# Kernel optimization log

Measured on AMD Instinct MI355X. Metric: run time of the kernel, lower is better.

Reference implementation:

```python
import jax, jax.numpy as jnp
import numpy as np

D = 1024   # embed_dim
H = 16     # n_heads
DH = D // H
B, N = 4, 1024


def setup_inputs() -> dict:
    key = jax.random.key(0)
    k0, k1, k2 = jax.random.split(key, 3)
    x = jax.random.normal(k0, (B, N, D), jnp.float32)
    # Per-head kqv Linear weights batched: each head maps D -> 2*D + D//H
    Wkqv = jax.random.normal(k1, (H, D, 2 * D + DH), jnp.float32) * 0.02
    bkqv = jnp.zeros((H, 2 * D + DH), jnp.float32)
    Wp = jax.random.normal(k2, (D, D), jnp.float32) * 0.02
    bp = jnp.zeros((D,), jnp.float32)
    return {"x": x, "Wkqv": Wkqv, "bkqv": bkqv, "Wp": Wp, "bp": bp}


def reference(x, Wkqv, bkqv, Wp, bp):
    Bm, Nm, Dm = x.shape
    # batched per-head projections: y[b,h,n,:] = x[b,n,:] @ Wkqv[h] + bkqv[h]
    y = jnp.einsum('bnd,hde->bhne', x, Wkqv) + bkqv[None, :, None, :]
    k = y[..., :Dm]          # [B,H,N,D]  (full embed_dim per head, as in source)
    q = y[..., Dm:2 * Dm]    # [B,H,N,D]
    v = y[..., 2 * Dm:]      # [B,H,N,DH]
    # attention_scores: q @ k^T / sqrt(D) -- scale uses FULL embed_dim (faithful)
    A = jnp.einsum('bhnd,bhmd->bhnm', q, k) / jnp.sqrt(jnp.float32(Dm))
    mask = jnp.tril(jnp.ones((Nm, Nm), dtype=bool))
    A = jnp.where(mask[None, None], A, -jnp.inf)
    A = jax.nn.softmax(A, axis=-1)
    sa = jnp.einsum('bhnm,bhmd->bnhd', A, v).reshape(Bm, Nm, Dm)
    return sa @ Wp + bp
```

## Files before the change

kernel.cpp:

```cpp
#include <hip/hip_runtime.h>
#include <hip/hip_bf16.h>

#define B_ 4
#define N_ 1024
#define D_ 1024
#define H_ 16
#define DH_ 64
#define E_ 2112
#define ROWS_ 4096

typedef __bf16 bf16_t;
typedef bf16_t bf16x4 __attribute__((ext_vector_type(4)));
typedef bf16_t bf16x8 __attribute__((ext_vector_type(8)));
typedef float f32x4 __attribute__((ext_vector_type(4)));

__device__ __forceinline__ void gload_lds16(const void* g, void* l) {
  __builtin_amdgcn_global_load_lds(
      (const __attribute__((address_space(1))) void*)g,
      (__attribute__((address_space(3))) void*)l, 16, 0, 0);
}

__global__ __launch_bounds__(256)
void prep_all(const float* __restrict__ x, const float* __restrict__ Wp,
              const float* __restrict__ W, const float* __restrict__ bkqv,
              bf16_t* __restrict__ xb, bf16_t* __restrict__ Wpt,
              bf16_t* __restrict__ Wvt, float* __restrict__ bqk) {
  __shared__ float smem[1056];
  const int bid = blockIdx.x;
  const int t = threadIdx.x;
  if (bid < 1024) {
    const int n4 = ROWS_ * D_ / 4;
    for (int i = bid * 256 + t; i < n4; i += 1024 * 256) {
      float4 v = ((const float4*)x)[i];
      bf16x4 o = {(bf16_t)v.x, (bf16_t)v.y, (bf16_t)v.z, (bf16_t)v.w};
      ((bf16x4*)xb)[i] = o;
    }
  } else if (bid < 2048) {
    const int id = bid - 1024;
    const int nt = id & 31, kt = id >> 5;
    const int tx = t & 31, ty = t >> 5;
    #pragma unroll
    for (int rr = 0; rr < 4; ++rr)
      smem[(rr * 8 + ty) * 33 + tx] =
          Wp[(size_t)(kt * 32 + rr * 8 + ty) * D_ + nt * 32 + tx];
    __syncthreads();
    #pragma unroll
    for (int rr = 0; rr < 4; ++rr)
      Wpt[(size_t)(nt * 32 + rr * 8 + ty) * D_ + kt * 32 + tx] =
          (bf16_t)smem[tx * 33 + rr * 8 + ty];
  } else if (bid < 3072) {
    const int id = bid - 2048;
    const int et = id & 1, dt = (id >> 1) & 31, h = id >> 6;
    const int tx = t & 31, ty = t >> 5;
    const float* Wh = W + (size_t)h * D_ * E_;
    #pragma unroll
    for (int rr = 0; rr < 4; ++rr) {
      int d = dt * 32 + rr * 8 + ty;
      int dh = et * 32 + tx;
      smem[(rr * 8 + ty) * 33 + tx] = Wh[(size_t)d * E_ + 2048 + dh];
    }
    __syncthreads();
    bf16_t* Wvo = Wvt + (size_t)h * DH_ * D_;
    #pragma unroll
    for (int rr = 0; rr < 4; ++rr) {
      int dh = et * 32 + rr * 8 + ty;
      int d = dt * 32 + tx;
      Wvo[(size_t)dh * D_ + d] = (bf16_t)smem[tx * 33 + rr * 8 + ty];
    }
  } else {
    const int h = bid - 3072;
    const float* bk = bkqv + h * E_;
    const float* bq = bk + 1024;
    float4 a = *(const float4*)(bk + t * 4);
    float4 b = *(const float4*)(bq + t * 4);
    smem[t] = a.x * b.x + a.y * b.y + a.z * b.z + a.w * b.w;
    __syncthreads();
    for (int st = 128; st > 0; st >>= 1) {
      if (t < st) smem[t] += smem[t + st];
      __syncthreads();
    }
    if (t == 0) bqk[h] = smem[0];
  }
}

__global__ __launch_bounds__(256)
void conv_wqk(const float* __restrict__ W, const float* __restrict__ bkqv,
              bf16_t* __restrict__ Wqb, bf16_t* __restrict__ Wkb,
              float* __restrict__ wqbk, float* __restrict__ wkbq) {
  const int db = blockIdx.x;
  const int h = blockIdx.y;
  const float* Wh = W + (size_t)h * D_ * E_;
  __shared__ float bq[1024], bk[1024];
  __shared__ float red[2][16][17];
  const int t = threadIdx.x;
  for (int i = t; i < 1024; i += 256) {
    bk[i] = bkqv[h * E_ + i];
    bq[i] = bkqv[h * E_ + 1024 + i];
  }
  __syncthreads();
  const int rt = t >> 4, ct = t & 15;
  const int d = db * 16 + rt;
  const float* rowp = Wh + (size_t)d * E_;
  float pk = 0.f, pq = 0.f;
  #pragma unroll
  for (int j = 0; j < 16; ++j) {
    int e4 = (ct + j * 16) * 4;
    float4 vk = *(const float4*)(rowp + e4);
    float4 vq = *(const float4*)(rowp + 1024 + e4);
    bf16x4 ok = {(bf16_t)vk.x, (bf16_t)vk.y, (bf16_t)vk.z, (bf16_t)vk.w};
    bf16x4 oq = {(bf16_t)vq.x, (bf16_t)vq.y, (bf16_t)vq.z, (bf16_t)vq.w};
    *(bf16x4*)(Wkb + ((size_t)h * 1024 + d) * 1024 + e4) = ok;
    *(bf16x4*)(Wqb + ((size_t)h * 1024 + d) * 1024 + e4) = oq;
    pk += vk.x * bq[e4] + vk.y * bq[e4 + 1] + vk.z * bq[e4 + 2] + vk.w * bq[e4 + 3];
    pq += vq.x * bk[e4] + vq.y * bk[e4 + 1] + vq.z * bk[e4 + 2] + vq.w * bk[e4 + 3];
  }
  red[0][rt][ct] = pk;
  red[1][rt][ct] = pq;
  __syncthreads();
  if (t < 32) {
    int which = t >> 4, r = t & 15;
    float s = 0.f;
    #pragma unroll
    for (int c2 = 0; c2 < 16; ++c2) s += red[which][r][c2];
    if (which == 0) wkbq[h * 1024 + db * 16 + r] = s;
    else            wqbk[h * 1024 + db * 16 + r] = s;
  }
}

__global__ __launch_bounds__(256)
void uv_kernel(const float* __restrict__ x, const float* __restrict__ bqk,
               const float* __restrict__ wqbk, const float* __restrict__ wkbq,
               float* __restrict__ u, float* __restrict__ v) {
  const int t = threadIdx.x;
  const int w = t >> 6, l = t & 63;
  const int rg = blockIdx.x * 4 + w;
  const int b = rg >> 10, n = rg & 1023;
  const float* xr = x + (size_t)rg * 1024 + l * 16;
  float4 xv0 = *(const float4*)(xr);
  float4 xv1 = *(const float4*)(xr + 4);
  float4 xv2 = *(const float4*)(xr + 8);
  float4 xv3 = *(const float4*)(xr + 12);
  #pragma unroll
  for (int h = 0; h < 16; ++h) {
    const float* wq = wqbk + h * 1024 + l * 16;
    const float* wk = wkbq + h * 1024 + l * 16;
    float4 q0 = *(const float4*)(wq);
    float4 q1 = *(const float4*)(wq + 4);
    float4 q2 = *(const float4*)(wq + 8);
    float4 q3 = *(const float4*)(wq + 12);
    float4 k0 = *(const float4*)(wk);
    float4 k1 = *(const float4*)(wk + 4);
    float4 k2 = *(const float4*)(wk + 8);
    float4 k3 = *(const float4*)(wk + 12);
    float au = xv0.x * q0.x + xv0.y * q0.y + xv0.z * q0.z + xv0.w * q0.w
             + xv1.x * q1.x + xv1.y * q1.y + xv1.z * q1.z + xv1.w * q1.w
             + xv2.x * q2.x + xv2.y * q2.y + xv2.z * q2.z + xv2.w * q2.w
             + xv3.x * q3.x + xv3.y * q3.y + xv3.z * q3.z + xv3.w * q3.w;
    float av = xv0.x * k0.x + xv0.y * k0.y + xv0.z * k0.z + xv0.w * k0.w
             + xv1.x * k1.x + xv1.y * k1.y + xv1.z * k1.z + xv1.w * k1.w
             + xv2.x * k2.x + xv2.y * k2.y + xv2.z * k2.z + xv2.w * k2.w
             + xv3.x * k3.x + xv3.y * k3.y + xv3.z * k3.z + xv3.w * k3.w;
    #pragma unroll
    for (int s = 1; s < 64; s <<= 1) {
      au += __shfl_xor(au, s);
      av += __shfl_xor(av, s);
    }
    if (l == 0) {
      int bh = b * 16 + h;
      u[(size_t)bh * 1024 + n] = au + bqk[h];
      v[(size_t)bh * 1024 + n] = av;
    }
  }
}

__global__ __launch_bounds__(256)
void v_gemm(const bf16_t* __restrict__ xb, const bf16_t* __restrict__ Wvt,
            const float* __restrict__ bkqv, bf16_t* __restrict__ Vt) {
  const int nt = blockIdx.x;
  const int h = blockIdx.y;
  const int t = threadIdx.x;
  const int w = t >> 6, l = t & 63, l15 = l & 15, lg = l >> 4;

  __shared__ bf16_t As2[64 * 64];
  __shared__ bf16_t Bs2[128 * 64];
  const bf16_t* Wvh = Wvt + (size_t)h * DH_ * D_;
  const bf16_t* Bn = xb + (size_t)nt * 128 * D_;

  f32x4 acc[4][2] = {};
  const int rswz = (l15 & 7) << 4;

  for (int kb = 0; kb < 16; ++kb) {
    __syncthreads();
    #pragma unroll
    for (int i = 0; i < 2; ++i) {
      int idx = t + i * 256;
      int row = idx >> 3, c = idx & 7;
      gload_lds16(Wvh + (size_t)row * D_ + kb * 64 + ((c ^ (row & 7)) << 3),
                  (char*)As2 + idx * 16);
    }
    #pragma unroll
    for (int i = 0; i < 4; ++i) {
      int idx = t + i * 256;
      int row = idx >> 3, c = idx & 7;
      gload_lds16(Bn + (size_t)row * D_ + kb * 64 + ((c ^ (row & 7)) << 3),
                  (char*)Bs2 + idx * 16);
    }
    __syncthreads();
    #pragma unroll
    for (int ks = 0; ks < 2; ++ks) {
      const int cswz = (ks * 64 + lg * 16) ^ rswz;
      bf16x8 a[4], b[2];
      #pragma unroll
      for (int mi = 0; mi < 4; ++mi)
        a[mi] = *(const bf16x8*)((const char*)As2 + (mi * 16 + l15) * 128 + cswz);
      #pragma unroll
      for (int ni = 0; ni < 2; ++ni)
        b[ni] = *(const bf16x8*)((const char*)Bs2 + (w * 32 + ni * 16 + l15) * 128 + cswz);
      #pragma unroll
      for (int mi = 0; mi < 4; ++mi)
        #pragma unroll
        for (int ni = 0; ni < 2; ++ni)
          acc[mi][ni] = __builtin_amdgcn_mfma_f32_16x16x32_bf16(a[mi], b[ni], acc[mi][ni], 0, 0, 0);
    }
  }

  #pragma unroll
  for (int mi = 0; mi < 4; ++mi)
    #pragma unroll
    for (int r = 0; r < 4; ++r) {
      int dh = mi * 16 + lg * 4 + r;
      float bias = bkqv[h * E_ + 2048 + dh];
      #pragma unroll
      for (int ni = 0; ni < 2; ++ni) {
        int nn = nt * 128 + w * 32 + ni * 16 + l15;
        int b = nn >> 10, n = nn & (N_ - 1);
        int bh = b * H_ + h;
        Vt[((size_t)bh * DH_ + dh) * N_ + n] = (bf16_t)(acc[mi][ni][r] + bias);
      }
    }
}

#define WV8 asm volatile("s_waitcnt vmcnt(8)" ::: "memory")
#define WV2 asm volatile("s_waitcnt vmcnt(2)" ::: "memory")
#define WV0 asm volatile("s_waitcnt vmcnt(0)" ::: "memory")
#define WNONE

__device__ __forceinline__ void mm256_core(const bf16_t* __restrict__ Ag,
                                           const bf16_t* __restrict__ Bg,
                                           bf16_t* lds, f32x4 (&acc)[8][4]) {
  char* Asp = (char*)lds;
  char* Bsp = (char*)lds + 65536;
  const int t = threadIdx.x;
  const int w = t >> 6, l = t & 63, l15 = l & 15, lg = l >> 4;
  const int wm = w >> 2, wn = w & 3;

  const int lr = l >> 3;
  const int scol = ((l & 7) ^ lr) << 3;
  const bf16_t* bS = Bg + (size_t)(w * 8 + lr) * 1024 + scol;
  const int idxA = w * 8 + lr;
  const bf16_t* aS0 = Ag + (size_t)((idxA >> 4) * 32 + (idxA & 15)) * 1024 + scol;
  const bf16_t* aS1 = aS0 + (size_t)128 * 1024;

#define STG_B(bufi, hh, ktv)                                                   \
  do {                                                                         \
    gload_lds16(bS + (size_t)((hh) * 128) * 1024 + (ktv) * 64,                 \
                Bsp + (bufi) * 32768 + (hh) * 16384 + w * 1024);               \
    gload_lds16(bS + (size_t)((hh) * 128 + 64) * 1024 + (ktv) * 64,            \
                Bsp + (bufi) * 32768 + (hh) * 16384 + 8192 + w * 1024);        \
  } while (0)
#define STG_A(bufi, hh, ktv)                                                   \
  do {                                                                         \
    gload_lds16(aS0 + (size_t)((hh) * 16) * 1024 + (ktv) * 64,                 \
                Asp + (bufi) * 32768 + (hh) * 16384 + w * 1024);               \
    gload_lds16(aS1 + (size_t)((hh) * 16) * 1024 + (ktv) * 64,                 \
                Asp + (bufi) * 32768 + (hh) * 16384 + 8192 + w * 1024);        \
  } while (0)

  STG_B(0, 0, 0); STG_B(0, 1, 0);
  STG_A(0, 0, 0); STG_A(0, 1, 0);
  STG_B(1, 0, 1); STG_B(1, 1, 1);
  STG_A(1, 0, 1);
  WV8;
  __builtin_amdgcn_s_barrier();

  const int rswz = (l15 & 7) << 4;
  const int bro = ((wn & 1) * 64 + l15) * 128;

#define TILE_STEP(KT, SA1, SB, SA0, W1, W3)                                    \
  {                                                                            \
    const int kb_ = (KT) & 1;                                                  \
    const char* Ab = Asp + kb_ * 32768;                                        \
    const char* Bb = Bsp + kb_ * 32768 + (wn >> 1) * 16384;                    \
    bf16x8 b0[4], b1[4];                                                       \
    {                                                                          \
      const int cs = (lg * 16) ^ rswz;                                         \
      bf16x8 a[4];                                                             \
      _Pragma("unroll") for (int ni = 0; ni < 4; ++ni)                         \
        b0[ni] = *(const bf16x8*)(Bb + bro + ni * 2048 + cs);                  \
      _Pragma("unroll") for (int q = 0; q < 4; ++q)                            \
        a[q] = *(const bf16x8*)(Ab + ((wm * 4 + q) * 16 + l15) * 128 + cs);    \
      if (SA1) STG_A(((KT) + 1) & 1, 1, (KT) + 1);                             \
      asm volatile("s_waitcnt lgkmcnt(0)" ::: "memory");                       \
      __builtin_amdgcn_s_setprio(1);                                           \
      _Pragma("unroll") for (int q = 0; q < 4; ++q)                            \
        _Pragma("unroll") for (int ni = 0; ni < 4; ++ni)                       \
          acc[2 * q][ni] = __builtin_amdgcn_mfma_f32_16x16x32_bf16(            \
              a[q], b0[ni], acc[2 * q][ni], 0, 0, 0);                          \
      __builtin_amdgcn_s_setprio(0);                                           \
      __builtin_amdgcn_s_barrier();                                            \
    }                                                                          \
    {                                                                          \
      const int cs = (64 + lg * 16) ^ rswz;                                    \
      bf16x8 a[4];                                                             \
      _Pragma("unroll") for (int ni = 0; ni < 4; ++ni)                         \
        b1[ni] = *(const bf16x8*)(Bb + bro + ni * 2048 + cs);                  \
      _Pragma("unroll") for (int q = 0; q < 4; ++q)                            \
        a[q] = *(const bf16x8*)(Ab + ((wm * 4 + q) * 16 + l15) * 128 + cs);    \
      asm volatile("s_waitcnt lgkmcnt(0)" ::: "memory");                       \
      __builtin_amdgcn_s_setprio(1);                                           \
      _Pragma("unroll") for (int q = 0; q < 4; ++q)                            \
        _Pragma("unroll") for (int ni = 0; ni < 4; ++ni)                       \
          acc[2 * q][ni] = __builtin_amdgcn_mfma_f32_16x16x32_bf16(            \
              a[q], b1[ni], acc[2 * q][ni], 0, 0, 0);                          \
      __builtin_amdgcn_s_setprio(0);                                           \
      W1;                                                                      \
      __builtin_amdgcn_s_barrier();                                            \
    }                                                                          \
    {                                                                          \
      const int cs = (lg * 16) ^ rswz;                                         \
      bf16x8 a[4];                                                             \
      _Pragma("unroll") for (int q = 0; q < 4; ++q)                            \
        a[q] = *(const bf16x8*)(Ab + 16384 + ((wm * 4 + q) * 16 + l15) * 128 + cs); \
      if (SB) { STG_B((KT) & 1, 0, (KT) + 2); STG_B((KT) & 1, 1, (KT) + 2); }  \
      asm volatile("s_waitcnt lgkmcnt(0)" ::: "memory");                       \
      __builtin_amdgcn_s_setprio(1);                                           \
      _Pragma("unroll") for (int q = 0; q < 4; ++q)                            \
        _Pragma("unroll") for (int ni = 0; ni < 4; ++ni)                       \
          acc[2 * q + 1][ni] = __builtin_amdgcn_mfma_f32_16x16x32_bf16(        \
              a[q], b0[ni], acc[2 * q + 1][ni], 0, 0, 0);                      \
      __builtin_amdgcn_s_setprio(0);                                           \
      __builtin_amdgcn_s_barrier();                                            \
    }                                                                          \
    {                                                                          \
      const int cs = (64 + lg * 16) ^ rswz;                                    \
      bf16x8 a[4];                                                             \
      _Pragma("unroll") for (int q = 0; q < 4; ++q)                            \
        a[q] = *(const bf16x8*)(Ab + 16384 + ((wm * 4 + q) * 16 + l15) * 128 + cs); \
      if (SA0) STG_A((KT) & 1, 0, (KT) + 2);                                   \
      asm volatile("s_waitcnt lgkmcnt(0)" ::: "memory");                       \
      __builtin_amdgcn_s_setprio(1);                                           \
      _Pragma("unroll") for (int q = 0; q < 4; ++q)                            \
        _Pragma("unroll") for (int ni = 0; ni < 4; ++ni)                       \
          acc[2 * q + 1][ni] = __builtin_amdgcn_mfma_f32_16x16x32_bf16(        \
              a[q], b1[ni], acc[2 * q + 1][ni], 0, 0, 0);                      \
      __builtin_amdgcn_s_setprio(0);                                           \
      W3;                                                                      \
      __builtin_amdgcn_s_barrier();                                            \
    }                                                                          \
  }

  for (int kt = 0; kt < 14; ++kt) TILE_STEP(kt, 1, 1, 1, WV8, WV8);
  TILE_STEP(14, 1, 0, 0, WV8, WV2);
  TILE_STEP(15, 0, 0, 0, WV0, WNONE);

#undef TILE_STEP
#undef STG_A
#undef STG_B
}

__device__ __forceinline__ int xchunk4(int colf) {
  int c = colf >> 2;
  return ((c ^ (c >> 3)) << 2) | (colf & 3);
}

__device__ __forceinline__ void epi256_bf16(f32x4 (&acc)[8][4], bf16_t* lds,
                                            bf16_t* dst) {
  const int t = threadIdx.x;
  const int l = t & 63, l15 = l & 15, lg = l >> 4;
  const int w = t >> 6;
  const int wm = w >> 2, wn = w & 3;
  float* Ct = (float*)lds;
  const int cpair = t & 31;
  const int p0 = xchunk4(cpair * 8);
  const int p1 = xchunk4(cpair * 8 + 4);
  #pragma unroll
  for (int s = 0; s < 4; ++s) {
    __syncthreads();
    #pragma unroll
    for (int m2 = 0; m2 < 2; ++m2)
      #pragma unroll
      for (int ni = 0; ni < 4; ++ni)
        #pragma unroll
        for (int r = 0; r < 4; ++r)
          Ct[(wm * 32 + m2 * 16 + lg * 4 + r) * 258 +
             xchunk4(wn * 64 + ni * 16 + l15)] = acc[2 * s + m2][ni][r];
    __syncthreads();
    #pragma unroll
    for (int it = 0; it < 4; ++it) {
      int row64 = (t >> 5) + it * 16;
      int wmq = row64 >> 5, m2q = (row64 >> 4) & 1, r16 = row64 & 15;
      int c8 = cpair * 8;
      const float* r0 = &Ct[row64 * 258 + p0];
      const float* r1 = &Ct[row64 * 258 + p1];
      bf16x8 o = {(bf16_t)r0[0], (bf16_t)r0[1], (bf16_t)r0[2], (bf16_t)r0[3],
                  (bf16_t)r1[0], (bf16_t)r1[1], (bf16_t)r1[2], (bf16_t)r1[3]};
      int lrow = wmq * 128 + (2 * s + m2q) * 16 + r16;
      *(bf16x8*)(dst + (size_t)lrow * 1024 + c8) = o;
    }
  }
}

__global__ __launch_bounds__(512)
void m_gemm(const bf16_t* __restrict__ Wkb, const bf16_t* __restrict__ Wqb,
            bf16_t* __restrict__ MT) {
  __shared__ bf16_t lds[65536];
  const int bid = blockIdx.x;
  const int mb = bid & 3, nb = (bid >> 2) & 3, h = bid >> 4;
  f32x4 acc[8][4] = {};
  mm256_core(Wkb + ((size_t)h * 1024 + mb * 256) * 1024,
             Wqb + ((size_t)h * 1024 + nb * 256) * 1024, lds, acc);
  epi256_bf16(acc, lds,
              MT + ((size_t)h * 1024 + mb * 256) * 1024 + nb * 256);
}

__global__ __launch_bounds__(512)
void t_gemm(const bf16_t* __restrict__ xb, const bf16_t* __restrict__ MT,
            bf16_t* __restrict__ T) {
  __shared__ bf16_t lds[65536];
  const int bid = blockIdx.x;
  const int lid = (bid & 7) * 128 + (bid >> 3);
  const int mb = lid & 15, nb = (lid >> 4) & 3, h = lid >> 6;
  f32x4 acc[8][4] = {};
  mm256_core(xb + (size_t)mb * 256 * 1024,
             MT + ((size_t)h * 1024 + nb * 256) * 1024, lds, acc);
  const int b = mb >> 2;
  const int bh = b * 16 + h;
  epi256_bf16(acc, lds,
              T + (size_t)bh * 1024 * 1024 + (size_t)((mb & 3) * 256) * 1024 +
                  nb * 256);
}

__global__ __launch_bounds__(512)
void s_gemm256(const bf16_t* __restrict__ T, const bf16_t* __restrict__ xb,
               const float* __restrict__ u, const float* __restrict__ v,
               bf16_t* __restrict__ Sg) {
  __shared__ bf16_t lds[65536];
  const int bid = blockIdx.x;
  const int lid = (bid & 7) * 80 + (bid >> 3);
  const int idx = lid % 10;
  const int bh = lid / 10;
  const int bb = bh >> 4;
  int qt = 0;
  while ((qt + 1) * (qt + 2) / 2 <= idx) ++qt;
  const int kt = idx - qt * (qt + 1) / 2;

  f32x4 acc[8][4] = {};
  mm256_core(T + (size_t)bh * 1024 * 1024 + (size_t)qt * 256 * 1024,
             xb + (size_t)bb * 1024 * 1024 + (size_t)kt * 256 * 1024, lds, acc);

  const int t = threadIdx.x;
  const int w = t >> 6, l = t & 63, l15 = l & 15, lg = l >> 4;
  const int wm = w >> 2, wn = w & 3;
  const float SCALE = 0.045084220027780106f;
  bf16_t* So = Sg + (((size_t)bh * 10 + idx) << 16);

  const float* ubh = u + (size_t)bh * 1024 + qt * 256;
  const float* vbh = v + (size_t)bh * 1024 + kt * 256;
  float vv[4];
  #pragma unroll
  for (int ni = 0; ni < 4; ++ni) vv[ni] = vbh[wn * 64 + ni * 16 + l15];

  #pragma unroll
  for (int mi = 0; mi < 8; ++mi)
    #pragma unroll
    for (int r = 0; r < 4; ++r) {
      int rl = wm * 128 + mi * 16 + lg * 4 + r;
      float uu = ubh[rl];
      #pragma unroll
      for (int ni = 0; ni < 4; ++ni) {
        int cl = wn * 64 + ni * 16 + l15;
        float z = (acc[mi][ni][r] + uu + vv[ni]) * SCALE;
        if (kt * 256 + cl > qt * 256 + rl) z = -1e30f;
        acc[mi][ni][r] = z;
      }
    }

  float* Ct = (float*)lds;
  const int cpair = t & 31;
  const int p0 = xchunk4(cpair * 8);
  const int p1 = xchunk4(cpair * 8 + 4);
  #pragma unroll
  for (int s = 0; s < 4; ++s) {
    __syncthreads();
    #pragma unroll
    for (int m2 = 0; m2 < 2; ++m2)
      #pragma unroll
      for (int ni = 0; ni < 4; ++ni)
        #pragma unroll
        for (int r = 0; r < 4; ++r)
          Ct[(wm * 32 + m2 * 16 + lg * 4 + r) * 258 +
             xchunk4(wn * 64 + ni * 16 + l15)] = acc[2 * s + m2][ni][r];
    __syncthreads();
    #pragma unroll
    for (int it = 0; it < 4; ++it) {
      int row64 = (t >> 5) + it * 16;
      int wmq = row64 >> 5, m2q = (row64 >> 4) & 1, r16 = row64 & 15;
      int c8 = cpair * 8;
      const float* r0 = &Ct[row64 * 258 + p0];
      const float* r1 = &Ct[row64 * 258 + p1];
      bf16x8 o = {(bf16_t)r0[0], (bf16_t)r0[1], (bf16_t)r0[2], (bf16_t)r0[3],
                  (bf16_t)r1[0], (bf16_t)r1[1], (bf16_t)r1[2], (bf16_t)r1[3]};
      int rl = wmq * 128 + (2 * s + m2q) * 16 + r16;
      *(bf16x8*)(So + (size_t)rl * 256 + c8) = o;
    }
  }
}

__global__ __launch_bounds__(256)
void softmax_pv(const bf16_t* __restrict__ Sg, const bf16_t* __restrict__ Vt,
                bf16_t* __restrict__ sa) {
  const int qt = blockIdx.x;
  const int bh = blockIdx.y;
  const int t = threadIdx.x;
  const int w = t >> 6, l = t & 63, l15 = l & 15, lg = l >> 4;
  const int b = bh >> 4, h = bh & 15;

  const int qrow = qt * 64 + w * 16 + l15;
  const int qt8 = qt >> 2;
  const bf16_t* Sbh = Sg + (((size_t)bh * 10) << 16);
  const bf16_t* Vh = Vt + (size_t)bh * DH_ * N_;

  f32x4 accO[4] = {};
  float m = -1e30f, lsum = 0.f;

  for (int j = 0; j <= qt; ++j) {
    const int jb = j * 64;
    const int tid = qt8 * (qt8 + 1) / 2 + (j >> 2);
    const bf16_t* Srow = Sbh + ((size_t)tid << 16) +
                         (size_t)(qrow & 255) * 256 + (jb & 255);

    bf16x8 h0 = *(const bf16x8*)(Srow + lg * 8);
    bf16x8 h1 = *(const bf16x8*)(Srow + 32 + lg * 8);
    float z[16];
    #pragma unroll
    for (int i = 0; i < 8; ++i) z[i] = (float)h0[i];
    #pragma unroll
    for (int i = 0; i < 8; ++i) z[8 + i] = (float)h1[i];

    float zm = z[0];
    #pragma unroll
    for (int i = 1; i < 16; ++i) zm = fmaxf(zm, z[i]);
    zm = fmaxf(zm, __shfl_xor(zm, 16));
    zm = fmaxf(zm, __shfl_xor(zm, 32));

    float mnew = fmaxf(m, zm);
    float scl = exp2f(m - mnew);
    m = mnew;

    float p[16];
    #pragma unroll
    for (int i = 0; i < 16; ++i) p[i] = exp2f(z[i] - mnew);

    float rs = 0.f;
    #pragma unroll
    for (int i = 0; i < 16; ++i) rs += p[i];
    rs += __shfl_xor(rs, 16);
    rs += __shfl_xor(rs, 32);
    lsum = lsum * scl + rs;

    float sclO[4];
    #pragma unroll
    for (int r = 0; r < 4; ++r) sclO[r] = __shfl(scl, lg * 4 + r);
    #pragma unroll
    for (int db = 0; db < 4; ++db)
      #pragma unroll
      for (int r = 0; r < 4; ++r) accO[db][r] *= sclO[r];

    bf16x8 pa0 = {(bf16_t)p[0], (bf16_t)p[1], (bf16_t)p[2], (bf16_t)p[3],
                  (bf16_t)p[4], (bf16_t)p[5], (bf16_t)p[6], (bf16_t)p[7]};
    bf16x8 pa1 = {(bf16_t)p[8], (bf16_t)p[9], (bf16_t)p[10], (bf16_t)p[11],
                  (bf16_t)p[12], (bf16_t)p[13], (bf16_t)p[14], (bf16_t)p[15]};

    #pragma unroll
    for (int db = 0; db < 4; ++db) {
      const bf16_t* vp = Vh + (size_t)(db * 16 + l15) * N_ + jb;
      bf16x8 vb0 = *(const bf16x8*)(vp + lg * 8);
      bf16x8 vb1 = *(const bf16x8*)(vp + 32 + lg * 8);
      accO[db] = __builtin_amdgcn_mfma_f32_16x16x32_bf16(pa0, vb0, accO[db], 0, 0, 0);
      accO[db] = __builtin_amdgcn_mfma_f32_16x16x32_bf16(pa1, vb1, accO[db], 0, 0, 0);
    }
  }

  float lO[4];
  #pragma unroll
  for (int r = 0; r < 4; ++r) lO[r] = __shfl(lsum, lg * 4 + r);

  #pragma unroll
  for (int db = 0; db < 4; ++db)
    #pragma unroll
    for (int r = 0; r < 4; ++r) {
      int row = qt * 64 + w * 16 + lg * 4 + r;
      int col = h * DH_ + db * 16 + l15;
      sa[((size_t)b * N_ + row) * D_ + col] = (bf16_t)(accO[db][r] / lO[r]);
    }
}

__global__ __launch_bounds__(256)
void out_gemm(const bf16_t* __restrict__ A, const bf16_t* __restrict__ Bt,
              const float* __restrict__ bp, float* __restrict__ out) {
  const int mb = blockIdx.x, nb = blockIdx.y;
  const int t = threadIdx.x;
  const int w = t >> 6, l = t & 63, l15 = l & 15, lg = l >> 4;
  const int wr = (w >> 1) * 64, wc = (w & 1) * 64;

  __shared__ bf16_t As[128 * 64];
  __shared__ bf16_t Bs[128 * 64];

  const int srow = w * 32 + (l >> 3);
  const int scol = (l & 7) * 8;
  const bf16_t* ag = A + (size_t)(mb * 128 + srow) * D_ + scol;
  const bf16_t* bg = Bt + (size_t)(nb * 128 + srow) * D_ + scol;
  char* asl = (char*)As + w * 4096;
  char* bsl = (char*)Bs + w * 4096;

  f32x4 acc[4][4] = {};

  for (int kb = 0; kb < 16; ++kb) {
    __syncthreads();
    #pragma unroll
    for (int i = 0; i < 4; ++i) {
      gload_lds16(ag + (size_t)i * 8 * D_ + kb * 64, asl + i * 1024);
      gload_lds16(bg + (size_t)i * 8 * D_ + kb * 64, bsl + i * 1024);
    }
    __syncthreads();
    #pragma unroll
    for (int ks = 0; ks < 2; ++ks) {
      bf16x8 a[4], b[4];
      #pragma unroll
      for (int mi = 0; mi < 4; ++mi)
        a[mi] = *(const bf16x8*)((const char*)As + (wr + mi * 16 + l15) * 128 + ks * 64 + lg * 16);
      #pragma unroll
      for (int ni = 0; ni < 4; ++ni)
        b[ni] = *(const bf16x8*)((const char*)Bs + (wc + ni * 16 + l15) * 128 + ks * 64 + lg * 16);
      #pragma unroll
      for (int mi = 0; mi < 4; ++mi)
        #pragma unroll
        for (int ni = 0; ni < 4; ++ni)
          acc[mi][ni] = __builtin_amdgcn_mfma_f32_16x16x32_bf16(a[mi], b[ni], acc[mi][ni], 0, 0, 0);
    }
  }

  #pragma unroll
  for (int ni = 0; ni < 4; ++ni) {
    int e = nb * 128 + wc + ni * 16 + l15;
    float bias = bp[e];
    #pragma unroll
    for (int mi = 0; mi < 4; ++mi)
      #pragma unroll
      for (int r = 0; r < 4; ++r) {
        int grow = mb * 128 + wr + mi * 16 + lg * 4 + r;
        out[(size_t)grow * D_ + e] = acc[mi][ni][r] + bias;
      }
  }
}

extern "C" void kernel_launch(void* const* d_in, const int* in_sizes, int n_in,
                              void* d_out, int out_size, void* d_ws, size_t ws_size,
                              hipStream_t stream) {
  const float* x    = (const float*)d_in[0];
  const float* Wkqv = (const float*)d_in[1];
  const float* bkqv = (const float*)d_in[2];
  const float* Wp   = (const float*)d_in[3];
  const float* bp   = (const float*)d_in[4];
  float* out = (float*)d_out;
  char* ws = (char*)d_ws;

  const size_t MB = 1 << 20;
  bf16_t* xb   = (bf16_t*)(ws);
  bf16_t* sa   = (bf16_t*)(ws + 8 * MB);
  bf16_t* Wpt  = (bf16_t*)(ws + 16 * MB);
  bf16_t* Vt   = (bf16_t*)(ws + 18 * MB);
  bf16_t* Wvt  = (bf16_t*)(ws + 26 * MB);
  bf16_t* MT   = (bf16_t*)(ws + 28 * MB);
  bf16_t* T    = (bf16_t*)(ws + 60 * MB);
  bf16_t* Wqb  = (bf16_t*)(ws + 188 * MB);
  bf16_t* Wkb  = (bf16_t*)(ws + 220 * MB);
  bf16_t* Sg   = (bf16_t*)(ws + 188 * MB);
  float*  u    = (float*) (ws + 268 * MB);
  float*  v    = (float*) (ws + 268 * MB + 256 * 1024);
  float*  wqbk = (float*) (ws + 268 * MB + 512 * 1024);
  float*  wkbq = (float*) (ws + 268 * MB + 576 * 1024);
  float*  bqk  = (float*) (ws + 268 * MB + 640 * 1024);

  hipLaunchKernelGGL(prep_all, dim3(3088), dim3(256), 0, stream,
                     x, Wp, Wkqv, bkqv, xb, Wpt, Wvt, bqk);
  hipLaunchKernelGGL(conv_wqk, dim3(64, 16), dim3(256), 0, stream,
                     Wkqv, bkqv, Wqb, Wkb, wqbk, wkbq);
  hipLaunchKernelGGL(uv_kernel, dim3(1024), dim3(256), 0, stream,
                     x, bqk, wqbk, wkbq, u, v);
  hipLaunchKernelGGL(v_gemm, dim3(32, 16), dim3(256), 0, stream,
                     xb, Wvt, bkqv, Vt);
  hipLaunchKernelGGL(m_gemm, dim3(256), dim3(512), 0, stream, Wkb, Wqb, MT);
  hipLaunchKernelGGL(t_gemm, dim3(1024), dim3(512), 0, stream, xb, MT, T);
  hipLaunchKernelGGL(s_gemm256, dim3(640), dim3(512), 0, stream,
                     T, xb, u, v, Sg);
  hipLaunchKernelGGL(softmax_pv, dim3(16, 64), dim3(256), 0, stream,
                     Sg, Vt, sa);
  hipLaunchKernelGGL(out_gemm, dim3(32, 8), dim3(256), 0, stream,
                     sa, Wpt, bp, out);
}
```

Before: 450.0 us.

## Merge prep kernels, fuse uv with v_gemm, restructure 256-tile GEMM pipeline

Folds conv_wqk into prep_all and merges uv_kernel with v_gemm into one launch, cutting the launch count from four to two and letting independent work share the GPU. The mm256_core main loop is restructured: all global-to-LDS staging for a k-tile is issued once after the compute barrier, LDS fragment reads are front-loaded with partial lgkmcnt waits, and fewer barriers are used per step. The s_gemm epilogue now reuses the shared epi256_bf16 helper with a row-stride parameter. The risk is less overlap of global loads with MFMA within a step and more LDS register pressure from holding extra fragments.

```diff
diff --git a/kernel.cpp b/kernel.cpp
--- a/kernel.cpp
+++ b/kernel.cpp
@@ -24,8 +24,10 @@
 void prep_all(const float* __restrict__ x, const float* __restrict__ Wp,
               const float* __restrict__ W, const float* __restrict__ bkqv,
               bf16_t* __restrict__ xb, bf16_t* __restrict__ Wpt,
-              bf16_t* __restrict__ Wvt, float* __restrict__ bqk) {
-  __shared__ float smem[1056];
+              bf16_t* __restrict__ Wvt, float* __restrict__ bqk,
+              bf16_t* __restrict__ Wqb, bf16_t* __restrict__ Wkb,
+              float* __restrict__ wqbk, float* __restrict__ wkbq) {
+  __shared__ float smem[2592];
   const int bid = blockIdx.x;
   const int t = threadIdx.x;
   if (bid < 1024) {
@@ -67,7 +69,7 @@
       int d = dt * 32 + tx;
       Wvo[(size_t)dh * D_ + d] = (bf16_t)smem[tx * 33 + rr * 8 + ty];
     }
-  } else {
+  } else if (bid < 3088) {
     const int h = bid - 3072;
     const float* bk = bkqv + h * E_;
     const float* bq = bk + 1024;
@@ -80,109 +82,103 @@
       __syncthreads();
     }
     if (t == 0) bqk[h] = smem[0];
+  } else {
+    const int id = bid - 3088;
+    const int db = id & 63, h = id >> 6;
+    const float* Wh = W + (size_t)h * D_ * E_;
+    float* bkL = smem;
+    float* bqL = smem + 1024;
+    float* red = smem + 2048;
+    for (int i = t; i < 1024; i += 256) {
+      bkL[i] = bkqv[h * E_ + i];
+      bqL[i] = bkqv[h * E_ + 1024 + i];
+    }
+    __syncthreads();
+    const int rt = t >> 4, ct = t & 15;
+    const int d = db * 16 + rt;
+    const float* rowp = Wh + (size_t)d * E_;
+    float pk = 0.f, pq = 0.f;
+    #pragma unroll
+    for (int j = 0; j < 16; ++j) {
+      int e4 = (ct + j * 16) * 4;
+      float4 vk = *(const float4*)(rowp + e4);
+      float4 vq = *(const float4*)(rowp + 1024 + e4);
+      bf16x4 ok = {(bf16_t)vk.x, (bf16_t)vk.y, (bf16_t)vk.z, (bf16_t)vk.w};
+      bf16x4 oq = {(bf16_t)vq.x, (bf16_t)vq.y, (bf16_t)vq.z, (bf16_t)vq.w};
+      *(bf16x4*)(Wkb + ((size_t)h * 1024 + d) * 1024 + e4) = ok;
+      *(bf16x4*)(Wqb + ((size_t)h * 1024 + d) * 1024 + e4) = oq;
+      pk += vk.x * bqL[e4] + vk.y * bqL[e4 + 1] + vk.z * bqL[e4 + 2] + vk.w * bqL[e4 + 3];
+      pq += vq.x * bkL[e4] + vq.y * bkL[e4 + 1] + vq.z * bkL[e4 + 2] + vq.w * bkL[e4 + 3];
+    }
+    red[0 * 272 + rt * 17 + ct] = pk;
+    red[1 * 272 + rt * 17 + ct] = pq;
+    __syncthreads();
+    if (t < 32) {
+      int which = t >> 4, r = t & 15;
+      float s = 0.f;
+      #pragma unroll
+      for (int c2 = 0; c2 < 16; ++c2) s += red[which * 272 + r * 17 + c2];
+      if (which == 0) wkbq[h * 1024 + db * 16 + r] = s;
+      else            wqbk[h * 1024 + db * 16 + r] = s;
+    }
   }
 }
 
 __global__ __launch_bounds__(256)
-void conv_wqk(const float* __restrict__ W, const float* __restrict__ bkqv,
-              bf16_t* __restrict__ Wqb, bf16_t* __restrict__ Wkb,
-              float* __restrict__ wqbk, float* __restrict__ wkbq) {
-  const int db = blockIdx.x;
-  const int h = blockIdx.y;
-  const float* Wh = W + (size_t)h * D_ * E_;
-  __shared__ float bq[1024], bk[1024];
-  __shared__ float red[2][16][17];
-  const int t = threadIdx.x;
-  for (int i = t; i < 1024; i += 256) {
-    bk[i] = bkqv[h * E_ + i];
-    bq[i] = bkqv[h * E_ + 1024 + i];
-  }
-  __syncthreads();
-  const int rt = t >> 4, ct = t & 15;
-  const int d = db * 16 + rt;
-  const float* rowp = Wh + (size_t)d * E_;
-  float pk = 0.f, pq = 0.f;
-  #pragma unroll
-  for (int j = 0; j < 16; ++j) {
-    int e4 = (ct + j * 16) * 4;
-    float4 vk = *(const float4*)(rowp + e4);
-    float4 vq = *(const float4*)(rowp + 1024 + e4);
-    bf16x4 ok = {(bf16_t)vk.x, (bf16_t)vk.y, (bf16_t)vk.z, (bf16_t)vk.w};
-    bf16x4 oq = {(bf16_t)vq.x, (bf16_t)vq.y, (bf16_t)vq.z, (bf16_t)vq.w};
-    *(bf16x4*)(Wkb + ((size_t)h * 1024 + d) * 1024 + e4) = ok;
-    *(bf16x4*)(Wqb + ((size_t)h * 1024 + d) * 1024 + e4) = oq;
-    pk += vk.x * bq[e4] + vk.y * bq[e4 + 1] + vk.z * bq[e4 + 2] + vk.w * bq[e4 + 3];
-    pq += vq.x * bk[e4] + vq.y * bk[e4 + 1] + vq.z * bk[e4 + 2] + vq.w * bk[e4 + 3];
-  }
-  red[0][rt][ct] = pk;
-  red[1][rt][ct] = pq;
-  __syncthreads();
-  if (t < 32) {
-    int which = t >> 4, r = t & 15;
-    float s = 0.f;
-    #pragma unroll
-    for (int c2 = 0; c2 < 16; ++c2) s += red[which][r][c2];
-    if (which == 0) wkbq[h * 1024 + db * 16 + r] = s;
-    else            wqbk[h * 1024 + db * 16 + r] = s;
-  }
-}
-
-__global__ __launch_bounds__(256)
-void uv_kernel(const float* __restrict__ x, const float* __restrict__ bqk,
-               const float* __restrict__ wqbk, const float* __restrict__ wkbq,
-               float* __restrict__ u, float* __restrict__ v) {
-  const int t = threadIdx.x;
-  const int w = t >> 6, l = t & 63;
-  const int rg = blockIdx.x * 4 + w;
-  const int b = rg >> 10, n = rg & 1023;
-  const float* xr = x + (size_t)rg * 1024 + l * 16;
-  float4 xv0 = *(const float4*)(xr);
-  float4 xv1 = *(const float4*)(xr + 4);
-  float4 xv2 = *(const float4*)(xr + 8);
-  float4 xv3 = *(const float4*)(xr + 12);
-  #pragma unroll
-  for (int h = 0; h < 16; ++h) {
-    const float* wq = wqbk + h * 1024 + l * 16;
-    const float* wk = wkbq + h * 1024 + l * 16;
-    float4 q0 = *(const float4*)(wq);
-    float4 q1 = *(const float4*)(wq + 4);
-    float4 q2 = *(const float4*)(wq + 8);
-    float4 q3 = *(const float4*)(wq + 12);
-    float4 k0 = *(const float4*)(wk);
-    float4 k1 = *(const float4*)(wk + 4);
-    float4 k2 = *(const float4*)(wk + 8);
-    float4 k3 = *(const float4*)(wk + 12);
-    float au = xv0.x * q0.x + xv0.y * q0.y + xv0.z * q0.z + xv0.w * q0.w
-             + xv1.x * q1.x + xv1.y * q1.y + xv1.z * q1.z + xv1.w * q1.w
-             + xv2.x * q2.x + xv2.y * q2.y + xv2.z * q2.z + xv2.w * q2.w
-             + xv3.x * q3.x + xv3.y * q3.y + xv3.z * q3.z + xv3.w * q3.w;
-    float av = xv0.x * k0.x + xv0.y * k0.y + xv0.z * k0.z + xv0.w * k0.w
-             + xv1.x * k1.x + xv1.y * k1.y + xv1.z * k1.z + xv1.w * k1.w
-             + xv2.x * k2.x + xv2.y * k2.y + xv2.z * k2.z + xv2.w * k2.w
-             + xv3.x * k3.x + xv3.y * k3.y + xv3.z * k3.z + xv3.w * k3.w;
-    #pragma unroll
-    for (int s = 1; s < 64; s <<= 1) {
-      au += __shfl_xor(au, s);
-      av += __shfl_xor(av, s);
-    }
-    if (l == 0) {
-      int bh = b * 16 + h;
-      u[(size_t)bh * 1024 + n] = au + bqk[h];
-      v[(size_t)bh * 1024 + n] = av;
-    }
-  }
-}
-
-__global__ __launch_bounds__(256)
-void v_gemm(const bf16_t* __restrict__ xb, const bf16_t* __restrict__ Wvt,
-            const float* __restrict__ bkqv, bf16_t* __restrict__ Vt) {
-  const int nt = blockIdx.x;
-  const int h = blockIdx.y;
-  const int t = threadIdx.x;
-  const int w = t >> 6, l = t & 63, l15 = l & 15, lg = l >> 4;
-
+void uv_v(const float* __restrict__ x, const float* __restrict__ bqk,
+          const float* __restrict__ wqbk, const float* __restrict__ wkbq,
+          float* __restrict__ u, float* __restrict__ v,
+          const bf16_t* __restrict__ xb, const bf16_t* __restrict__ Wvt,
+          const float* __restrict__ bkqv, bf16_t* __restrict__ Vt) {
   __shared__ bf16_t As2[64 * 64];
   __shared__ bf16_t Bs2[128 * 64];
+  const int bid = blockIdx.x;
+  const int t = threadIdx.x;
+  if (bid < 1024) {
+    const int w = t >> 6, l = t & 63;
+    const int rg = bid * 4 + w;
+    const int b = rg >> 10, n = rg & 1023;
+    const float* xr = x + (size_t)rg * 1024 + l * 16;
+    float4 xv0 = *(const float4*)(xr);
+    float4 xv1 = *(const float4*)(xr + 4);
+    float4 xv2 = *(const float4*)(xr + 8);
+    float4 xv3 = *(const float4*)(xr + 12);
+    #pragma unroll
+    for (int h = 0; h < 16; ++h) {
+      const float* wq = wqbk + h * 1024 + l * 16;
+      const float* wk = wkbq + h * 1024 + l * 16;
+      float4 q0 = *(const float4*)(wq);
+      float4 q1 = *(const float4*)(wq + 4);
+      float4 q2 = *(const float4*)(wq + 8);
+      float4 q3 = *(const float4*)(wq + 12);
+      float4 k0 = *(const float4*)(wk);
+      float4 k1 = *(const float4*)(wk + 4);
+      float4 k2 = *(const float4*)(wk + 8);
+      float4 k3 = *(const float4*)(wk + 12);
+      float au = xv0.x * q0.x + xv0.y * q0.y + xv0.z * q0.z + xv0.w * q0.w
+               + xv1.x * q1.x + xv1.y * q1.y + xv1.z * q1.z + xv1.w * q1.w
+               + xv2.x * q2.x + xv2.y * q2.y + xv2.z * q2.z + xv2.w * q2.w
+               + xv3.x * q3.x + xv3.y * q3.y + xv3.z * q3.z + xv3.w * q3.w;
+      float av = xv0.x * k0.x + xv0.y * k0.y + xv0.z * k0.z + xv0.w * k0.w
+               + xv1.x * k1.x + xv1.y * k1.y + xv1.z * k1.z + xv1.w * k1.w
+               + xv2.x * k2.x + xv2.y * k2.y + xv2.z * k2.z + xv2.w * k2.w
+               + xv3.x * k3.x + xv3.y * k3.y + xv3.z * k3.z + xv3.w * k3.w;
+      #pragma unroll
+      for (int s = 1; s < 64; s <<= 1) {
+        au += __shfl_xor(au, s);
+        av += __shfl_xor(av, s);
+      }
+      if (l == 0) {
+        int bh = b * 16 + h;
+        u[(size_t)bh * 1024 + n] = au + bqk[h];
+        v[(size_t)bh * 1024 + n] = av;
+      }
+    }
+    return;
+  }
+  const int id = bid - 1024;
+  const int nt = id & 31, h = id >> 5;
+  const int w = t >> 6, l = t & 63, l15 = l & 15, lg = l >> 4;
   const bf16_t* Wvh = Wvt + (size_t)h * DH_ * D_;
   const bf16_t* Bn = xb + (size_t)nt * 128 * D_;
 
@@ -239,11 +235,6 @@
       }
     }
 }
-
-#define WV8 asm volatile("s_waitcnt vmcnt(8)" ::: "memory")
-#define WV2 asm volatile("s_waitcnt vmcnt(2)" ::: "memory")
-#define WV0 asm volatile("s_waitcnt vmcnt(0)" ::: "memory")
-#define WNONE
 
 __device__ __forceinline__ void mm256_core(const bf16_t* __restrict__ Ag,
                                            const bf16_t* __restrict__ Bg,
@@ -261,111 +252,100 @@
   const bf16_t* aS0 = Ag + (size_t)((idxA >> 4) * 32 + (idxA & 15)) * 1024 + scol;
   const bf16_t* aS1 = aS0 + (size_t)128 * 1024;
 
-#define STG_B(bufi, hh, ktv)                                                   \
+#define STG_ALL(bufi, ktv)                                                     \
   do {                                                                         \
-    gload_lds16(bS + (size_t)((hh) * 128) * 1024 + (ktv) * 64,                 \
-                Bsp + (bufi) * 32768 + (hh) * 16384 + w * 1024);               \
-    gload_lds16(bS + (size_t)((hh) * 128 + 64) * 1024 + (ktv) * 64,            \
-                Bsp + (bufi) * 32768 + (hh) * 16384 + 8192 + w * 1024);        \
+    gload_lds16(bS + (size_t)0 * 1024 + (ktv) * 64,                            \
+                Bsp + (bufi) * 32768 + w * 1024);                              \
+    gload_lds16(bS + (size_t)64 * 1024 + (ktv) * 64,                           \
+                Bsp + (bufi) * 32768 + 8192 + w * 1024);                       \
+    gload_lds16(bS + (size_t)128 * 1024 + (ktv) * 64,                          \
+                Bsp + (bufi) * 32768 + 16384 + w * 1024);                      \
+    gload_lds16(bS + (size_t)192 * 1024 + (ktv) * 64,                          \
+                Bsp + (bufi) * 32768 + 16384 + 8192 + w * 1024);               \
+    gload_lds16(aS0 + (size_t)0 * 1024 + (ktv) * 64,                           \
+                Asp + (bufi) * 32768 + w * 1024);                              \
+    gload_lds16(aS1 + (size_t)0 * 1024 + (ktv) * 64,                           \
+                Asp + (bufi) * 32768 + 8192 + w * 1024);                       \
+    gload_lds16(aS0 + (size_t)16 * 1024 + (ktv) * 64,                          \
+                Asp + (bufi) * 32768 + 16384 + w * 1024);                      \
+    gload_lds16(aS1 + (size_t)16 * 1024 + (ktv) * 64,                          \
+                Asp + (bufi) * 32768 + 16384 + 8192 + w * 1024);               \
   } while (0)
-#define STG_A(bufi, hh, ktv)                                                   \
-  do {                                                                         \
-    gload_lds16(aS0 + (size_t)((hh) * 16) * 1024 + (ktv) * 64,                 \
-                Asp + (bufi) * 32768 + (hh) * 16384 + w * 1024);               \
-    gload_lds16(aS1 + (size_t)((hh) * 16) * 1024 + (ktv) * 64,                 \
-                Asp + (bufi) * 32768 + (hh) * 16384 + 8192 + w * 1024);        \
-  } while (0)
-
-  STG_B(0, 0, 0); STG_B(0, 1, 0);
-  STG_A(0, 0, 0); STG_A(0, 1, 0);
-  STG_B(1, 0, 1); STG_B(1, 1, 1);
-  STG_A(1, 0, 1);
-  WV8;
+
+  STG_ALL(0, 0);
+  STG_ALL(1, 1);
+  asm volatile("s_waitcnt vmcnt(8)" ::: "memory");
   __builtin_amdgcn_s_barrier();
 
   const int rswz = (l15 & 7) << 4;
   const int bro = ((wn & 1) * 64 + l15) * 128;
 
-#define TILE_STEP(KT, SA1, SB, SA0, W1, W3)                                    \
+#define TILE_STEP(KT, DO_STG, WVW, DO_ENDBAR)                                  \
   {                                                                            \
-    const int kb_ = (KT) & 1;                                                  \
-    const char* Ab = Asp + kb_ * 32768;                                        \
-    const char* Bb = Bsp + kb_ * 32768 + (wn >> 1) * 16384;                    \
-    bf16x8 b0[4], b1[4];                                                       \
-    {                                                                          \
-      const int cs = (lg * 16) ^ rswz;                                         \
-      bf16x8 a[4];                                                             \
+    const char* Ab = Asp + ((KT) & 1) * 32768;                                 \
+    const char* Bb = Bsp + ((KT) & 1) * 32768 + (wn >> 1) * 16384;             \
+    const int cs0 = (lg * 16) ^ rswz;                                          \
+    const int cs1 = (64 + lg * 16) ^ rswz;                                     \
+    bf16x8 b0[4], b1[4], ae0[4], ae1[4], ao0[4], ao1[4];                       \
+    _Pragma("unroll") for (int ni = 0; ni < 4; ++ni)                           \
+      b0[ni] = *(const bf16x8*)(Bb + bro + ni * 2048 + cs0);                   \
+    _Pragma("unroll") for (int q = 0; q < 4; ++q)                              \
+      ae0[q] = *(const bf16x8*)(Ab + ((wm * 4 + q) * 16 + l15) * 128 + cs0);   \
+    _Pragma("unroll") for (int ni = 0; ni < 4; ++ni)                           \
+      b1[ni] = *(const bf16x8*)(Bb + bro + ni * 2048 + cs1);                   \
+    _Pragma("unroll") for (int q = 0; q < 4; ++q)                              \
+      ae1[q] = *(const bf16x8*)(Ab + ((wm * 4 + q) * 16 + l15) * 128 + cs1);   \
+    asm volatile("s_waitcnt lgkmcnt(8)" ::: "memory");                         \
+    __builtin_amdgcn_s_setprio(1);                                             \
+    _Pragma("unroll") for (int q = 0; q < 4; ++q)                              \
       _Pragma("unroll") for (int ni = 0; ni < 4; ++ni)                         \
-        b0[ni] = *(const bf16x8*)(Bb + bro + ni * 2048 + cs);                  \
-      _Pragma("unroll") for (int q = 0; q < 4; ++q)                            \
-        a[q] = *(const bf16x8*)(Ab + ((wm * 4 + q) * 16 + l15) * 128 + cs);    \
-      if (SA1) STG_A(((KT) + 1) & 1, 1, (KT) + 1);                             \
-      asm volatile("s_waitcnt lgkmcnt(0)" ::: "memory");                       \
-      __builtin_amdgcn_s_setprio(1);                                           \
-      _Pragma("unroll") for (int q = 0; q < 4; ++q)                            \
-        _Pragma("unroll") for (int ni = 0; ni < 4; ++ni)                       \
-          acc[2 * q][ni] = __builtin_amdgcn_mfma_f32_16x16x32_bf16(            \
-              a[q], b0[ni], acc[2 * q][ni], 0, 0, 0);                          \
-      __builtin_amdgcn_s_setprio(0);                                           \
-      __builtin_amdgcn_s_barrier();                                            \
-    }                                                                          \
-    {                                                                          \
-      const int cs = (64 + lg * 16) ^ rswz;                                    \
-      bf16x8 a[4];                                                             \
+        acc[2 * q][ni] = __builtin_amdgcn_mfma_f32_16x16x32_bf16(              \
+            ae0[q], b0[ni], acc[2 * q][ni], 0, 0, 0);                          \
+    __builtin_amdgcn_s_setprio(0);                                             \
+    _Pragma("unroll") for (int q = 0; q < 4; ++q)                              \
+      ao0[q] = *(const bf16x8*)(Ab + 16384 + ((wm * 4 + q) * 16 + l15) * 128 + cs0); \
+    asm volatile("s_waitcnt lgkmcnt(4)" ::: "memory");                         \
+    __builtin_amdgcn_s_setprio(1);                                             \
+    _Pragma("unroll") for (int q = 0; q < 4; ++q)                              \
       _Pragma("unroll") for (int ni = 0; ni < 4; ++ni)                         \
-        b1[ni] = *(const bf16x8*)(Bb + bro + ni * 2048 + cs);                  \
-      _Pragma("unroll") for (int q = 0; q < 4; ++q)                            \
-        a[q] = *(const bf16x8*)(Ab + ((wm * 4 + q) * 16 + l15) * 128 + cs);    \
-      asm volatile("s_waitcnt lgkmcnt(0)" ::: "memory");                       \
-      __builtin_amdgcn_s_setprio(1);                                           \
-      _Pragma("unroll") for (int q = 0; q < 4; ++q)                            \
-        _Pragma("unroll") for (int ni = 0; ni < 4; ++ni)                       \
-          acc[2 * q][ni] = __builtin_amdgcn_mfma_f32_16x16x32_bf16(            \
-              a[q], b1[ni], acc[2 * q][ni], 0, 0, 0);                          \
-      __builtin_amdgcn_s_setprio(0);                                           \
-      W1;                                                                      \
-      __builtin_amdgcn_s_barrier();                                            \
-    }                                                                          \
-    {                                                                          \
-      const int cs = (lg * 16) ^ rswz;                                         \
-      bf16x8 a[4];                                                             \
-      _Pragma("unroll") for (int q = 0; q < 4; ++q)                            \
-        a[q] = *(const bf16x8*)(Ab + 16384 + ((wm * 4 + q) * 16 + l15) * 128 + cs); \
-      if (SB) { STG_B((KT) & 1, 0, (KT) + 2); STG_B((KT) & 1, 1, (KT) + 2); }  \
-      asm volatile("s_waitcnt lgkmcnt(0)" ::: "memory");                       \
-      __builtin_amdgcn_s_setprio(1);                                           \
-      _Pragma("unroll") for (int q = 0; q < 4; ++q)                            \
-        _Pragma("unroll") for (int ni = 0; ni < 4; ++ni)                       \
-          acc[2 * q + 1][ni] = __builtin_amdgcn_mfma_f32_16x16x32_bf16(        \
-              a[q], b0[ni], acc[2 * q + 1][ni], 0, 0, 0);                      \
-      __builtin_amdgcn_s_setprio(0);                                           \
-      __builtin_amdgcn_s_barrier();                                            \
-    }                                                                          \
-    {                                                                          \
-      const int cs = (64 + lg * 16) ^ rswz;                                    \
-      bf16x8 a[4];                                                             \
-      _Pragma("unroll") for (int q = 0; q < 4; ++q)                            \
-        a[q] = *(const bf16x8*)(Ab + 16384 + ((wm * 4 + q) * 16 + l15) * 128 + cs); \
-      if (SA0) STG_A((KT) & 1, 0, (KT) + 2);                                   \
-      asm volatile("s_waitcnt lgkmcnt(0)" ::: "memory");                       \
-      __builtin_amdgcn_s_setprio(1);                                           \
-      _Pragma("unroll") for (int q = 0; q < 4; ++q)                            \
-        _Pragma("unroll") for (int ni = 0; ni < 4; ++ni)                       \
-          acc[2 * q + 1][ni] = __builtin_amdgcn_mfma_f32_16x16x32_bf16(        \
-              a[q], b1[ni], acc[2 * q + 1][ni], 0, 0, 0);                      \
-      __builtin_amdgcn_s_setprio(0);                                           \
-      W3;                                                                      \
-      __builtin_amdgcn_s_barrier();                                            \
-    }                                                                          \
-  }
-
-  for (int kt = 0; kt < 14; ++kt) TILE_STEP(kt, 1, 1, 1, WV8, WV8);
-  TILE_STEP(14, 1, 0, 0, WV8, WV2);
-  TILE_STEP(15, 0, 0, 0, WV0, WNONE);
+        acc[2 * q][ni] = __builtin_amdgcn_mfma_f32_16x16x32_bf16(              \
+            ae1[q], b1[ni], acc[2 * q][ni], 0, 0, 0);                          \
+    __builtin_amdgcn_s_setprio(0);                                             \
+    _Pragma("unroll") for (int q = 0; q < 4; ++q)                              \
+      ao1[q] = *(const bf16x8*)(Ab + 16384 + ((wm * 4 + q) * 16 + l15) * 128 + cs1); \
+    asm volatile("s_waitcnt lgkmcnt(4)" ::: "memory");                         \
+    __builtin_amdgcn_s_setprio(1);                                             \
+    _Pragma("unroll") for (int q = 0; q < 4; ++q)                              \
+      _Pragma("unroll") for (int ni = 0; ni < 4; ++ni)                         \
+        acc[2 * q + 1][ni] = __builtin_amdgcn_mfma_f32_16x16x32_bf16(          \
+            ao0[q], b0[ni], acc[2 * q + 1][ni], 0, 0, 0);                      \
+    __builtin_amdgcn_s_setprio(0);                                             \
+    asm volatile("s_waitcnt lgkmcnt(0)" ::: "memory");                         \
+    __builtin_amdgcn_s_setprio(1);                                             \
+    _Pragma("unroll") for (int q = 0; q < 4; ++q)                              \
+      _Pragma("unroll") for (int ni = 0; ni < 4; ++ni)                         \
+        acc[2 * q + 1][ni] = __builtin_amdgcn_mfma_f32_16x16x32_bf16(          \
+            ao1[q], b1[ni], acc[2 * q + 1][ni], 0, 0, 0);                      \
+    __builtin_amdgcn_s_setprio(0);                                             \
+    __builtin_amdgcn_s_barrier();                                              \
+    if (DO_STG) STG_ALL((KT) & 1, (KT) + 2);                                   \
+    WVW;                                                                       \
+    if (DO_ENDBAR) __builtin_amdgcn_s_barrier();                               \
+  }
+
+#define WV8_ asm volatile("s_waitcnt vmcnt(8)" ::: "memory")
+#define WV0_ asm volatile("s_waitcnt vmcnt(0)" ::: "memory")
+#define WN_
+
+  for (int kt = 0; kt < 14; ++kt) TILE_STEP(kt, 1, WV8_, 1);
+  TILE_STEP(14, 0, WV0_, 1);
+  TILE_STEP(15, 0, WN_, 0);
 
 #undef TILE_STEP
-#undef STG_A
-#undef STG_B
+#undef STG_ALL
+#undef WV8_
+#undef WV0_
+#undef WN_
 }
 
 __device__ __forceinline__ int xchunk4(int colf) {
@@ -374,7 +354,7 @@
 }
 
 __device__ __forceinline__ void epi256_bf16(f32x4 (&acc)[8][4], bf16_t* lds,
-                                            bf16_t* dst) {
+                                            bf16_t* dst, int rowstride) {
   const int t = threadIdx.x;
   const int l = t & 63, l15 = l & 15, lg = l >> 4;
   const int w = t >> 6;
@@ -405,7 +385,7 @@
       bf16x8 o = {(bf16_t)r0[0], (bf16_t)r0[1], (bf16_t)r0[2], (bf16_t)r0[3],
                   (bf16_t)r1[0], (bf16_t)r1[1], (bf16_t)r1[2], (bf16_t)r1[3]};
       int lrow = wmq * 128 + (2 * s + m2q) * 16 + r16;
-      *(bf16x8*)(dst + (size_t)lrow * 1024 + c8) = o;
+      *(bf16x8*)(dst + (size_t)lrow * rowstride + c8) = o;
     }
   }
 }
@@ -420,7 +400,7 @@
   mm256_core(Wkb + ((size_t)h * 1024 + mb * 256) * 1024,
              Wqb + ((size_t)h * 1024 + nb * 256) * 1024, lds, acc);
   epi256_bf16(acc, lds,
-              MT + ((size_t)h * 1024 + mb * 256) * 1024 + nb * 256);
+              MT + ((size_t)h * 1024 + mb * 256) * 1024 + nb * 256, 1024);
 }
 
 __global__ __launch_bounds__(512)
@@ -437,7 +417,7 @@
   const int bh = b * 16 + h;
   epi256_bf16(acc, lds,
               T + (size_t)bh * 1024 * 1024 + (size_t)((mb & 3) * 256) * 1024 +
-                  nb * 256);
+                  nb * 256, 1024);
 }
 
 __global__ __launch_bounds__(512)
@@ -485,35 +465,7 @@
       }
     }
 
-  float* Ct = (float*)lds;
-  const int cpair = t & 31;
-  const int p0 = xchunk4(cpair * 8);
-  const int p1 = xchunk4(cpair * 8 + 4);
-  #pragma unroll
-  for (int s = 0; s < 4; ++s) {
-    __syncthreads();
-    #pragma unroll
-    for (int m2 = 0; m2 < 2; ++m2)
-      #pragma unroll
-      for (int ni = 0; ni < 4; ++ni)
-        #pragma unroll
-        for (int r = 0; r < 4; ++r)
-          Ct[(wm * 32 + m2 * 16 + lg * 4 + r) * 258 +
-             xchunk4(wn * 64 + ni * 16 + l15)] = acc[2 * s + m2][ni][r];
-    __syncthreads();
-    #pragma unroll
-    for (int it = 0; it < 4; ++it) {
-      int row64 = (t >> 5) + it * 16;
-      int wmq = row64 >> 5, m2q = (row64 >> 4) & 1, r16 = row64 & 15;
-      int c8 = cpair * 8;
-      const float* r0 = &Ct[row64 * 258 + p0];
-      const float* r1 = &Ct[row64 * 258 + p1];
-      bf16x8 o = {(bf16_t)r0[0], (bf16_t)r0[1], (bf16_t)r0[2], (bf16_t)r0[3],
-                  (bf16_t)r1[0], (bf16_t)r1[1], (bf16_t)r1[2], (bf16_t)r1[3]};
-      int rl = wmq * 128 + (2 * s + m2q) * 16 + r16;
-      *(bf16x8*)(So + (size_t)rl * 256 + c8) = o;
-    }
-  }
+  epi256_bf16(acc, lds, So, 256);
 }
 
 __global__ __launch_bounds__(256)
@@ -692,14 +644,11 @@
   float*  wkbq = (float*) (ws + 268 * MB + 576 * 1024);
   float*  bqk  = (float*) (ws + 268 * MB + 640 * 1024);
 
-  hipLaunchKernelGGL(prep_all, dim3(3088), dim3(256), 0, stream,
-                     x, Wp, Wkqv, bkqv, xb, Wpt, Wvt, bqk);
-  hipLaunchKernelGGL(conv_wqk, dim3(64, 16), dim3(256), 0, stream,
-                     Wkqv, bkqv, Wqb, Wkb, wqbk, wkbq);
-  hipLaunchKernelGGL(uv_kernel, dim3(1024), dim3(256), 0, stream,
-                     x, bqk, wqbk, wkbq, u, v);
-  hipLaunchKernelGGL(v_gemm, dim3(32, 16), dim3(256), 0, stream,
-                     xb, Wvt, bkqv, Vt);
+  hipLaunchKernelGGL(prep_all, dim3(4112), dim3(256), 0, stream,
+                     x, Wp, Wkqv, bkqv, xb, Wpt, Wvt, bqk,
+                     Wqb, Wkb, wqbk, wkbq);
+  hipLaunchKernelGGL(uv_v, dim3(1536), dim3(256), 0, stream,
+                     x, bqk, wqbk, wkbq, u, v, xb, Wvt, bkqv, Vt);
   hipLaunchKernelGGL(m_gemm, dim3(256), dim3(512), 0, stream, Wkb, Wqb, MT);
   hipLaunchKernelGGL(t_gemm, dim3(1024), dim3(512), 0, stream, xb, MT, T);
   hipLaunchKernelGGL(s_gemm256, dim3(640), dim3(512), 0, stream,
```

Measured after the change: 480.3 us. 1.07x slower.
